# Kernel optimization log

Measured on AMD Instinct MI355X. Metric: run time of the kernel, lower is better.

Reference implementation:

```python
import jax, jax.numpy as jnp
import numpy as np

KERNEL_SIZE_FACTOR = 0.1
SIGMA = 3.0


def _determine_kernel_size(feature_map_size):
    size = int(feature_map_size * KERNEL_SIZE_FACTOR)
    return size if size % 2 == 1 else size + 1


def _gaussian_kernel_2d(size, sigma):
    # matches cv2.getGaussianKernel for sigma > 0: exp(-(i-c)^2/(2*sigma^2)), L1-normalized
    ax = jnp.arange(size, dtype=jnp.float32) - (size - 1) / 2.0
    k1 = jnp.exp(-(ax * ax) / (2.0 * sigma * sigma))
    k1 = k1 / jnp.sum(k1)
    return jnp.outer(k1, k1)  # [size, size]


def setup_inputs() -> dict:
    key = jax.random.key(0)
    k1, k2 = jax.random.split(key)
    feature_map = jax.random.normal(k1, (16, 64, 224, 224), dtype=jnp.float32)
    points = jax.random.uniform(k2, (16, 1024, 2), dtype=jnp.float32)
    return {"feature_map": feature_map, "points": points}


def reference(feature_map, points):
    B, C, H, W = feature_map.shape
    N = points.shape[1]
    ks = _determine_kernel_size(min(H, W))
    half = ks // 2
    kernel = _gaussian_kernel_2d(ks, SIGMA)

    # Boundary clipping in the original == scatter full kernel into a padded map, then crop.
    Hp, Wp = H + 2 * half, W + 2 * half

    x = (points[..., 0] * W).astype(jnp.int32)  # [B, N], floor of nonneg
    y = (points[..., 1] * H).astype(jnp.int32)  # [B, N]

    d = jnp.arange(ks, dtype=jnp.int32)
    # top-left corner in padded coords: (y - half) + half = y
    rows = y[:, :, None, None] + d[None, None, :, None]  # [B, N, ks, 1]
    cols = x[:, :, None, None] + d[None, None, None, :]  # [B, N, 1, ks]
    b = jnp.arange(B, dtype=jnp.int32)[:, None, None, None]
    flat_idx = ((b * Hp + rows) * Wp + cols).reshape(-1)  # [B*N*ks*ks]

    vals = jnp.broadcast_to(kernel, (B, N, ks, ks)).reshape(-1)
    sal = jnp.zeros(B * Hp * Wp, dtype=jnp.float32).at[flat_idx].add(vals)
    sal = sal.reshape(B, Hp, Wp)[:, half:half + H, half:half + W]
    return sal
```

## Files before the change

### kernel.cpp

```cpp
#include <hip/hip_runtime.h>
#include <math.h>

#define BB   16
#define HH   224
#define WW   224
#define NPTS 1024
#define KS   23
#define HALF 11
#define SIGMA2_2 18.0f

__device__ __forceinline__ void gauss_weights(float* w) {
    float s = 0.0f;
#pragma unroll
    for (int t = 0; t < KS; ++t) {
        float ax = (float)(t - HALF);
        float v = __expf(-(ax * ax) / SIGMA2_2);
        w[t] = v;
        s += v;
    }
    float inv = 1.0f / s;
#pragma unroll
    for (int t = 0; t < KS; ++t) w[t] *= inv;
}

__global__ void scatter_counts(const float* __restrict__ pts, float* __restrict__ cnt) {
    int idx = blockIdx.x * blockDim.x + threadIdx.x;
    if (idx >= BB * NPTS) return;
    int b = idx / NPTS;
    float px = pts[2 * idx + 0];
    float py = pts[2 * idx + 1];
    int x = (int)(px * (float)WW);
    int y = (int)(py * (float)HH);
    if ((unsigned)x >= WW || (unsigned)y >= HH) return;
    atomicAdd(&cnt[(b * HH + y) * WW + x], 1.0f);
}

__global__ void hconv(const float* __restrict__ cnt, float* __restrict__ tmp) {
    int idx = blockIdx.x * blockDim.x + threadIdx.x;
    if (idx >= BB * HH * WW) return;
    float w[KS];
    gauss_weights(w);
    int j = idx % WW;
    int rowbase = idx - j;
    float acc = 0.0f;
#pragma unroll
    for (int t = 0; t < KS; ++t) {
        int x = j + t - HALF;
        float v = ((unsigned)x < (unsigned)WW) ? cnt[rowbase + x] : 0.0f;
        acc = fmaf(v, w[t], acc);
    }
    tmp[idx] = acc;
}

__global__ void vconv(const float* __restrict__ tmp, float* __restrict__ out) {
    int idx = blockIdx.x * blockDim.x + threadIdx.x;
    if (idx >= BB * HH * WW) return;
    float w[KS];
    gauss_weights(w);
    int j = idx % WW;
    int rem = idx / WW;
    int i = rem % HH;
    int b = rem / HH;
    const float* base = tmp + (size_t)b * HH * WW + j;
    float acc = 0.0f;
#pragma unroll
    for (int t = 0; t < KS; ++t) {
        int y = i + t - HALF;
        float v = ((unsigned)y < (unsigned)HH) ? base[(size_t)y * WW] : 0.0f;
        acc = fmaf(v, w[t], acc);
    }
    out[idx] = acc;
}

extern "C" void kernel_launch(void* const* d_in, const int* in_sizes, int n_in,
                              void* d_out, int out_size, void* d_ws, size_t ws_size,
                              hipStream_t stream) {
    const float* pts = (const float*)d_in[1];
    float* out = (float*)d_out;

    const int PIX = BB * HH * WW;
    float* cnt = (float*)d_ws;
    float* tmp = cnt + PIX;

    hipMemsetAsync(cnt, 0, (size_t)PIX * sizeof(float), stream);

    scatter_counts<<<(BB * NPTS + 255) / 256, 256, 0, stream>>>(pts, cnt);
    hconv<<<(PIX + 255) / 256, 256, 0, stream>>>(cnt, tmp);
    vconv<<<(PIX + 255) / 256, 256, 0, stream>>>(tmp, out);
}
```

Measured before the change: 241.8 us.

## Fuse memset, scatter, and separable convolution into one cooperative kernel

Replaces the memset plus three kernel launches with a single cooperative persistent kernel that zeroes counts, scatters points, then runs the horizontal and vertical passes, separated by grid-wide syncs. The aim is to remove launch and inter-kernel gaps and to compute the Gaussian weights once per thread. In exchange it adds three grid barriers and a fixed grid of 1024 blocks using strided loops. If the cooperative launch fails, it falls back to the original path.

```diff
diff --git a/kernel.cpp b/kernel.cpp
--- a/kernel.cpp
+++ b/kernel.cpp
@@ -1,5 +1,8 @@
 #include <hip/hip_runtime.h>
+#include <hip/hip_cooperative_groups.h>
 #include <math.h>
+
+namespace cg = cooperative_groups;
 
 #define BB   16
 #define HH   224
@@ -8,6 +11,11 @@
 #define KS   23
 #define HALF 11
 #define SIGMA2_2 18.0f
+#define PIX  (BB * HH * WW)
+
+#define GRID_BLOCKS 1024
+#define BLOCK 256
+#define NTHREADS (GRID_BLOCKS * BLOCK)
 
 __device__ __forceinline__ void gauss_weights(float* w) {
     float s = 0.0f;
@@ -21,6 +29,65 @@
     float inv = 1.0f / s;
 #pragma unroll
     for (int t = 0; t < KS; ++t) w[t] *= inv;
+}
+
+__global__ __launch_bounds__(BLOCK, 4) void fused(const float* __restrict__ pts,
+                                                  float* __restrict__ out,
+                                                  float* __restrict__ cnt,
+                                                  float* __restrict__ tmp) {
+    cg::grid_group grid = cg::this_grid();
+    const int tid = blockIdx.x * BLOCK + threadIdx.x;
+
+    {
+        float4 z = make_float4(0.f, 0.f, 0.f, 0.f);
+        float4* c4 = (float4*)cnt;
+        for (int i = tid; i < PIX / 4; i += NTHREADS) c4[i] = z;
+    }
+    grid.sync();
+
+    if (tid < BB * NPTS) {
+        int b = tid >> 10;
+        float px = pts[2 * tid + 0];
+        float py = pts[2 * tid + 1];
+        int x = (int)(px * (float)WW);
+        int y = (int)(py * (float)HH);
+        if ((unsigned)x < (unsigned)WW && (unsigned)y < (unsigned)HH)
+            atomicAdd(&cnt[(b * HH + y) * WW + x], 1.0f);
+    }
+    grid.sync();
+
+    float w[KS];
+    gauss_weights(w);
+
+    for (int idx = tid; idx < PIX; idx += NTHREADS) {
+        int j = idx % WW;
+        int rowbase = idx - j;
+        float acc = 0.0f;
+#pragma unroll
+        for (int t = 0; t < KS; ++t) {
+            int x = j + t - HALF;
+            float v = ((unsigned)x < (unsigned)WW) ? cnt[rowbase + x] : 0.0f;
+            acc = fmaf(v, w[t], acc);
+        }
+        tmp[idx] = acc;
+    }
+    grid.sync();
+
+    for (int idx = tid; idx < PIX; idx += NTHREADS) {
+        int j = idx % WW;
+        int rem = idx / WW;
+        int i = rem % HH;
+        int b = rem / HH;
+        const float* base = tmp + (size_t)b * HH * WW + j;
+        float acc = 0.0f;
+#pragma unroll
+        for (int t = 0; t < KS; ++t) {
+            int y = i + t - HALF;
+            float v = ((unsigned)y < (unsigned)HH) ? base[(size_t)y * WW] : 0.0f;
+            acc = fmaf(v, w[t], acc);
+        }
+        out[idx] = acc;
+    }
 }
 
 __global__ void scatter_counts(const float* __restrict__ pts, float* __restrict__ cnt) {
@@ -78,13 +145,17 @@
     const float* pts = (const float*)d_in[1];
     float* out = (float*)d_out;
 
-    const int PIX = BB * HH * WW;
     float* cnt = (float*)d_ws;
     float* tmp = cnt + PIX;
 
-    hipMemsetAsync(cnt, 0, (size_t)PIX * sizeof(float), stream);
-
-    scatter_counts<<<(BB * NPTS + 255) / 256, 256, 0, stream>>>(pts, cnt);
-    hconv<<<(PIX + 255) / 256, 256, 0, stream>>>(cnt, tmp);
-    vconv<<<(PIX + 255) / 256, 256, 0, stream>>>(tmp, out);
+    void* args[] = {(void*)&pts, (void*)&out, (void*)&cnt, (void*)&tmp};
+    hipError_t err = hipLaunchCooperativeKernel((const void*)fused,
+                                                dim3(GRID_BLOCKS), dim3(BLOCK),
+                                                args, 0, stream);
+    if (err != hipSuccess) {
+        hipMemsetAsync(cnt, 0, (size_t)PIX * sizeof(float), stream);
+        scatter_counts<<<(BB * NPTS + 255) / 256, 256, 0, stream>>>(pts, cnt);
+        hconv<<<(PIX + 255) / 256, 256, 0, stream>>>(cnt, tmp);
+        vconv<<<(PIX + 255) / 256, 256, 0, stream>>>(tmp, out);
+    }
 }
```

After: 505.8 us. 109% more time.

## Fuse scatter and separable Gaussian convolution into one tiled shared-memory kernel

Applied to the files above, without the earlier changes.

Replaces the memset, global atomic scatter, horizontal conv and vertical conv kernels with one kernel per 32x32 output tile. Each block rebuilds the point-count map for its haloed tile in shared memory by scanning all 1024 points of its batch, then runs both conv passes from LDS and writes the output once. This removes the global count and intermediate buffers, their memory traffic and three extra launches. In exchange every block rereads all points of its batch and does some redundant halo work.

```diff
diff --git a/kernel.cpp b/kernel.cpp
--- a/kernel.cpp
+++ b/kernel.cpp
@@ -8,6 +8,13 @@
 #define KS   23
 #define HALF 11
 #define SIGMA2_2 18.0f
+
+#define TH 32
+#define TW 32
+#define IN_H (TH + 2 * HALF)
+#define IN_W (TW + 2 * HALF)
+#define TILES_X (WW / TW)
+#define TILES_PER_B (TILES_X * (HH / TH))
 
 __device__ __forceinline__ void gauss_weights(float* w) {
     float s = 0.0f;
@@ -23,53 +30,63 @@
     for (int t = 0; t < KS; ++t) w[t] *= inv;
 }
 
-__global__ void scatter_counts(const float* __restrict__ pts, float* __restrict__ cnt) {
-    int idx = blockIdx.x * blockDim.x + threadIdx.x;
-    if (idx >= BB * NPTS) return;
-    int b = idx / NPTS;
-    float px = pts[2 * idx + 0];
-    float py = pts[2 * idx + 1];
-    int x = (int)(px * (float)WW);
-    int y = (int)(py * (float)HH);
-    if ((unsigned)x >= WW || (unsigned)y >= HH) return;
-    atomicAdd(&cnt[(b * HH + y) * WW + x], 1.0f);
-}
+__global__ __launch_bounds__(256) void saliency_fused(const float* __restrict__ pts,
+                                                      float* __restrict__ out) {
+    __shared__ float cnt[IN_H * IN_W];
+    __shared__ float hbuf[IN_H * TW];
 
-__global__ void hconv(const float* __restrict__ cnt, float* __restrict__ tmp) {
-    int idx = blockIdx.x * blockDim.x + threadIdx.x;
-    if (idx >= BB * HH * WW) return;
+    const int blk = blockIdx.x;
+    const int b   = blk / TILES_PER_B;
+    const int t49 = blk % TILES_PER_B;
+    const int r0  = (t49 / TILES_X) * TH;
+    const int c0  = (t49 % TILES_X) * TW;
+    const int gr0 = r0 - HALF;
+    const int gc0 = c0 - HALF;
+    const int tid = threadIdx.x;
+
+    for (int i = tid; i < IN_H * IN_W; i += 256) cnt[i] = 0.0f;
+    __syncthreads();
+
+    {
+        const float* pb = pts + (size_t)b * NPTS * 2;
+        for (int p = tid; p < NPTS; p += 256) {
+            float px = pb[2 * p + 0];
+            float py = pb[2 * p + 1];
+            int x = (int)(px * (float)WW);
+            int y = (int)(py * (float)HH);
+            if ((unsigned)x < (unsigned)WW && (unsigned)y < (unsigned)HH) {
+                int lx = x - gc0;
+                int ly = y - gr0;
+                if ((unsigned)lx < (unsigned)IN_W && (unsigned)ly < (unsigned)IN_H)
+                    atomicAdd(&cnt[ly * IN_W + lx], 1.0f);
+            }
+        }
+    }
+    __syncthreads();
+
     float w[KS];
     gauss_weights(w);
-    int j = idx % WW;
-    int rowbase = idx - j;
-    float acc = 0.0f;
+
+    for (int i = tid; i < IN_H * TW; i += 256) {
+        int r = i / TW;
+        int c = i % TW;
+        const float* row = &cnt[r * IN_W + c];
+        float acc = 0.0f;
 #pragma unroll
-    for (int t = 0; t < KS; ++t) {
-        int x = j + t - HALF;
-        float v = ((unsigned)x < (unsigned)WW) ? cnt[rowbase + x] : 0.0f;
-        acc = fmaf(v, w[t], acc);
+        for (int t = 0; t < KS; ++t) acc = fmaf(row[t], w[t], acc);
+        hbuf[r * TW + c] = acc;
     }
-    tmp[idx] = acc;
-}
+    __syncthreads();
 
-__global__ void vconv(const float* __restrict__ tmp, float* __restrict__ out) {
-    int idx = blockIdx.x * blockDim.x + threadIdx.x;
-    if (idx >= BB * HH * WW) return;
-    float w[KS];
-    gauss_weights(w);
-    int j = idx % WW;
-    int rem = idx / WW;
-    int i = rem % HH;
-    int b = rem / HH;
-    const float* base = tmp + (size_t)b * HH * WW + j;
-    float acc = 0.0f;
+    for (int i = tid; i < TH * TW; i += 256) {
+        int r = i / TW;
+        int c = i % TW;
+        const float* col = &hbuf[r * TW + c];
+        float acc = 0.0f;
 #pragma unroll
-    for (int t = 0; t < KS; ++t) {
-        int y = i + t - HALF;
-        float v = ((unsigned)y < (unsigned)HH) ? base[(size_t)y * WW] : 0.0f;
-        acc = fmaf(v, w[t], acc);
+        for (int t = 0; t < KS; ++t) acc = fmaf(col[t * TW], w[t], acc);
+        out[((size_t)b * HH + (r0 + r)) * WW + (c0 + c)] = acc;
     }
-    out[idx] = acc;
 }
 
 extern "C" void kernel_launch(void* const* d_in, const int* in_sizes, int n_in,
@@ -78,13 +95,5 @@
     const float* pts = (const float*)d_in[1];
     float* out = (float*)d_out;
 
-    const int PIX = BB * HH * WW;
-    float* cnt = (float*)d_ws;
-    float* tmp = cnt + PIX;
-
-    hipMemsetAsync(cnt, 0, (size_t)PIX * sizeof(float), stream);
-
-    scatter_counts<<<(BB * NPTS + 255) / 256, 256, 0, stream>>>(pts, cnt);
-    hconv<<<(PIX + 255) / 256, 256, 0, stream>>>(cnt, tmp);
-    vconv<<<(PIX + 255) / 256, 256, 0, stream>>>(tmp, out);
+    saliency_fused<<<BB * TILES_PER_B, 256, 0, stream>>>(pts, out);
 }
```

Result: faster. 233.6 us (-3.4%).
